# Kernel tuning notes

Measured on AMD Instinct MI355X. Metric: run time of the kernel, lower is better.

Reference implementation:

```python
import jax, jax.numpy as jnp
import numpy as np

N = 50000
E = 800000
D_IN = 128
D_HID = 128
D_EMB = 128
N_CLS = 3
EPS = 0.0  # GINConv default eps, not trainable here
LRELU_SLOPE = 0.2


def setup_inputs() -> dict:
    key = jax.random.key(0)
    ks = jax.random.split(key, 12)
    x = jax.random.normal(ks[0], (N, D_IN), dtype=jnp.float32)
    edge_index = jax.random.randint(ks[1], (2, E), 0, N, dtype=jnp.int64)
    node_label = jnp.zeros((10000, 1, N_CLS), dtype=jnp.float32)
    node_index = jax.random.randint(ks[2], (10000,), 0, N, dtype=jnp.int64)
    def lin(k, fan_in, fan_out):
        kw, kb = jax.random.split(k)
        bound = 1.0 / np.sqrt(fan_in)
        W = jax.random.uniform(kw, (fan_out, fan_in), minval=-bound, maxval=bound, dtype=jnp.float32)
        b = jax.random.uniform(kb, (fan_out,), minval=-bound, maxval=bound, dtype=jnp.float32)
        return W, b
    W1, b1 = lin(ks[3], D_IN, D_HID)
    W2, b2 = lin(ks[4], D_HID, D_HID)
    W3, b3 = lin(ks[5], D_HID, D_EMB)
    Wout, bout = lin(ks[6], D_EMB, N_CLS)
    return {"x": x, "edge_index": edge_index, "node_label": node_label,
            "node_index": node_index, "W1": W1, "b1": b1, "W2": W2, "b2": b2,
            "W3": W3, "b3": b3, "Wout": Wout, "bout": bout}


def gin_conv(x, src, dst, W, b):
    # h = Linear(x); out = relu(scatter_add(h[src] -> dst) + (1+eps)*h)
    h = x @ W.T + b                                   # [N, F_out]
    agg = jax.ops.segment_sum(h[src], dst, num_segments=N)
    return jax.nn.relu(agg + (1.0 + EPS) * h)


def leaky_relu(x):
    return jnp.where(x >= 0, x, LRELU_SLOPE * x)


def reference(x, edge_index, node_label, node_index, W1, b1, W2, b2, W3, b3, Wout, bout):
    src, dst = edge_index[0], edge_index[1]
    h = leaky_relu(gin_conv(x, src, dst, W1, b1))
    h = leaky_relu(gin_conv(h, src, dst, W2, b2))
    h = leaky_relu(gin_conv(h, src, dst, W3, b3))
    x_embed = h                                       # [N, D_EMB]
    output = h @ Wout.T + bout                        # [N, N_CLS]
    node_output = output[node_index]                  # [M, N_CLS]
    ypred = jnp.argmax(output, axis=1)                # [N]
    y_nodepred = ypred[node_index]                    # [M]
    return (x_embed, node_output, ypred, y_nodepred)
```

## Files before the change

### kernel.cpp

```cpp
#include <hip/hip_runtime.h>

#define NN 50000
#define EE 800000
#define D 128
#define NCLS 3
#define MIDX 10000
#define NB 196
#define CHUNK 4096
#define HIST_WGS 98
#define CONV_WGS 25000

typedef unsigned int uint32;
typedef unsigned short ushort16;
typedef __attribute__((ext_vector_type(8))) short short8;
typedef __attribute__((ext_vector_type(4))) float f32x4;

__device__ __forceinline__ ushort16 f2bf(float f) {
    uint32 u = __float_as_uint(f);
    u = (u + 0x7fffu + ((u >> 16) & 1u)) >> 16;
    return (ushort16)u;
}
__device__ __forceinline__ float bflo(uint32 packed) {
    return __uint_as_float(packed << 16);
}
__device__ __forceinline__ float bfhi(uint32 packed) {
    return __uint_as_float(packed & 0xFFFF0000u);
}

__device__ __forceinline__ void gather_rows(const uint32* __restrict__ h,
                                            const int* __restrict__ esrc,
                                            int beg, int end, int lane,
                                            float& a0, float& a1) {
    int i = beg;
    for (; i + 16 <= end; i += 16) {
        int s[16];
        uint32 q[16];
#pragma unroll
        for (int k = 0; k < 16; ++k) s[k] = esrc[i + k];
#pragma unroll
        for (int k = 0; k < 16; ++k) q[k] = h[(long long)s[k] * (D / 2) + lane];
        float t0a = 0.f, t0b = 0.f, t1a = 0.f, t1b = 0.f;
#pragma unroll
        for (int k = 0; k < 16; k += 2) {
            t0a += bflo(q[k]);     t1a += bfhi(q[k]);
            t0b += bflo(q[k + 1]); t1b += bfhi(q[k + 1]);
        }
        a0 += t0a + t0b;
        a1 += t1a + t1b;
    }
    for (; i + 4 <= end; i += 4) {
        int s[4];
        uint32 q[4];
#pragma unroll
        for (int k = 0; k < 4; ++k) s[k] = esrc[i + k];
#pragma unroll
        for (int k = 0; k < 4; ++k) q[k] = h[(long long)s[k] * (D / 2) + lane];
        a0 += (bflo(q[0]) + bflo(q[1])) + (bflo(q[2]) + bflo(q[3]));
        a1 += (bfhi(q[0]) + bfhi(q[1])) + (bfhi(q[2]) + bfhi(q[3]));
    }
    for (; i < end; ++i) {
        const uint32 q = h[(long long)esrc[i] * (D / 2) + lane];
        a0 += bflo(q);
        a1 += bfhi(q);
    }
}


__global__ __launch_bounds__(256) void prep_hist(const float* __restrict__ x0,
                                                 const float* __restrict__ W1,
                                                 const float* __restrict__ W2,
                                                 const float* __restrict__ W3,
                                                 const int* __restrict__ dst,
                                                 ushort16* __restrict__ xbf,
                                                 ushort16* __restrict__ Wbf,
                                                 int* __restrict__ hpart) {
    const int t = threadIdx.x;
    if (blockIdx.x < CONV_WGS) {
        const int i = blockIdx.x * 256 + t;
        xbf[i] = f2bf(x0[i]);
        if (i < D * D) {
            Wbf[i] = f2bf(W1[i]);
            Wbf[i + D * D] = f2bf(W2[i]);
            Wbf[i + 2 * D * D] = f2bf(W3[i]);
        }
    } else {
        __shared__ int hcnt[256];
        const int b = blockIdx.x - CONV_WGS;
        hcnt[t] = 0;
        __syncthreads();
        const int e0 = b * 8192;
        const int e1 = (e0 + 8192 < EE) ? e0 + 8192 : EE;
        for (int s = e0 + t; s < e1; s += 256) atomicAdd(&hcnt[dst[s] >> 8], 1);
        __syncthreads();
        hpart[b * 256 + t] = hcnt[t];
    }
}

__global__ void coarse_scan(const int* __restrict__ hpart, int* __restrict__ bstart,
                            int* __restrict__ bcursor, int* __restrict__ rowptr) {
    __shared__ int s[256];
    const int t = threadIdx.x;
    int v = 0;
    if (t < NB)
        for (int w = 0; w < HIST_WGS; ++w) v += hpart[w * 256 + t];
    s[t] = v;
    __syncthreads();
    for (int off = 1; off < 256; off <<= 1) {
        const int add = (t >= off) ? s[t - off] : 0;
        __syncthreads();
        s[t] += add;
        __syncthreads();
    }
    const int excl = s[t] - v;
    if (t < NB) {
        bstart[t] = excl;
        bcursor[t * 16] = excl;
    }
    if (t == NB - 1) bstart[NB] = excl + v;
    if (t == 0) rowptr[NN] = EE;
}

__global__ __launch_bounds__(256) void fill_coarse(const int* __restrict__ src,
                                                   const int* __restrict__ dst,
                                                   int* __restrict__ bcursor,
                                                   int* __restrict__ espacked) {
    __shared__ int hcnt[256];
    __shared__ int hbase[256];
    const int t = threadIdx.x;
    const int e0 = blockIdx.x * CHUNK;
    const int e1 = (e0 + CHUNK < EE) ? e0 + CHUNK : EE;
    hcnt[t] = 0;
    __syncthreads();
    for (int s = e0 + t; s < e1; s += 256) atomicAdd(&hcnt[dst[s] >> 8], 1);
    __syncthreads();
    if (t < NB) {
        const int c = hcnt[t];
        hbase[t] = c ? atomicAdd(&bcursor[t * 16], c) : 0;
    }
    hcnt[t] = 0;
    __syncthreads();
    for (int s = e0 + t; s < e1; s += 256) {
        const int d = dst[s];
        const int b = d >> 8;
        const int r = atomicAdd(&hcnt[b], 1);
        espacked[hbase[b] + r] = (src[s] << 8) | (d & 255);
    }
}

__global__ __launch_bounds__(256) void bucket_scatter(const int* __restrict__ espacked,
                                                      const int* __restrict__ bstart,
                                                      int* __restrict__ rowptr,
                                                      int* __restrict__ esrc) {
    __shared__ int cnt[256];
    __shared__ int sc[256];
    __shared__ int cur[256];
    const int b = blockIdx.x;
    const int t = threadIdx.x;
    const int n0 = b * 256;
    const int seg0 = bstart[b];
    const int seg1 = bstart[b + 1];
    cnt[t] = 0;
    __syncthreads();
    for (int s = seg0 + t; s < seg1; s += 256) atomicAdd(&cnt[espacked[s] & 255], 1);
    __syncthreads();
    const int v = cnt[t];
    sc[t] = v;
    __syncthreads();
    for (int off = 1; off < 256; off <<= 1) {
        const int add = (t >= off) ? sc[t - off] : 0;
        __syncthreads();
        sc[t] += add;
        __syncthreads();
    }
    const int excl = seg0 + sc[t] - v;
    if (n0 + t < NN) rowptr[n0 + t] = excl;
    cur[t] = excl;
    __syncthreads();
    for (int s = seg0 + t; s < seg1; s += 256) {
        const int p = espacked[s];
        const int pos = atomicAdd(&cur[p & 255], 1);
        esrc[pos] = p >> 8;
    }
}


__global__ __launch_bounds__(256) void linear_mfma(const ushort16* __restrict__ x,
                                                   const ushort16* __restrict__ Wbf,
                                                   const float* __restrict__ bias,
                                                   ushort16* __restrict__ h) {
    const int wave = threadIdx.x >> 6;
    const int lane = threadIdx.x & 63;
    const int m0 = blockIdx.x * 64 + wave * 16;
    if (m0 >= NN) return;
    const int lr = lane & 15;
    const int lk = (lane >> 4) * 8;

    f32x4 acc[8] = {};
#pragma unroll
    for (int k4 = 0; k4 < 4; ++k4) {
        const int kb = k4 * 32 + lk;
        const short8 af = *(const short8*)(x + (long long)(m0 + lr) * D + kb);
#pragma unroll
        for (int nt = 0; nt < 8; ++nt) {
            const short8 bfrag = *(const short8*)(Wbf + (nt * 16 + lr) * D + kb);
            acc[nt] = __builtin_amdgcn_mfma_f32_16x16x32_bf16(af, bfrag, acc[nt], 0, 0, 0);
        }
    }
    const int rbase = m0 + (lane >> 4) * 4;
#pragma unroll
    for (int nt = 0; nt < 8; ++nt) {
        const int f = nt * 16 + lr;
        const float bb = bias[f];
#pragma unroll
        for (int r = 0; r < 4; ++r)
            h[(long long)(rbase + r) * D + f] = f2bf(acc[nt][r] + bb);
    }
}


__global__ __launch_bounds__(256) void agg_linear(const uint32* __restrict__ h,
                                                  const int* __restrict__ rowptr,
                                                  const int* __restrict__ esrc,
                                                  const ushort16* __restrict__ Wbf,
                                                  const float* __restrict__ bias,
                                                  ushort16* __restrict__ hnext) {
    __shared__ uint32 xs[16][68];
    const int wave = threadIdx.x >> 6;
    const int lane = threadIdx.x & 63;
    const int m0 = blockIdx.x * 16;

#pragma unroll
    for (int j = 0; j < 4; ++j) {
        const int row = wave * 4 + j;
        const int node = __builtin_amdgcn_readfirstlane(m0 + row);
        const int beg = rowptr[node];
        const int end = rowptr[node + 1];
        const uint32 p = h[(long long)node * (D / 2) + lane];
        float acc0 = bflo(p), acc1 = bfhi(p);
        gather_rows(h, esrc, beg, end, lane, acc0, acc1);
        xs[row][lane] = ((uint32)f2bf(fmaxf(acc1, 0.f)) << 16) |
                        (uint32)f2bf(fmaxf(acc0, 0.f));
    }
    __syncthreads();

    const int lr = lane & 15;
    const int lk = (lane >> 4) * 8;
    f32x4 acc[2] = {};
#pragma unroll
    for (int k4 = 0; k4 < 4; ++k4) {
        const int kb = k4 * 32 + lk;
        const short8 af = *(const short8*)&xs[lr][kb >> 1];
#pragma unroll
        for (int f = 0; f < 2; ++f) {
            const int ft = wave * 2 + f;
            const short8 bfrag = *(const short8*)(Wbf + (ft * 16 + lr) * D + kb);
            acc[f] = __builtin_amdgcn_mfma_f32_16x16x32_bf16(af, bfrag, acc[f], 0, 0, 0);
        }
    }
    const int rbase = m0 + (lane >> 4) * 4;
#pragma unroll
    for (int f = 0; f < 2; ++f) {
        const int col = (wave * 2 + f) * 16 + lr;
        const float bb = bias[col];
#pragma unroll
        for (int r = 0; r < 4; ++r)
            hnext[(long long)(rbase + r) * D + col] = f2bf(acc[f][r] + bb);
    }
}


__global__ __launch_bounds__(256) void agg_head(const uint32* __restrict__ h,
                                                const int* __restrict__ rowptr,
                                                const int* __restrict__ esrc,
                                                float* __restrict__ xe,
                                                const float* __restrict__ Wout,
                                                const float* __restrict__ bout,
                                                float* __restrict__ logits,
                                                float* __restrict__ ypred) {
    const int wave = threadIdx.x >> 6;
    const int lane = threadIdx.x & 63;
    const int node = __builtin_amdgcn_readfirstlane(blockIdx.x * 4 + wave);
    if (node >= NN) return;
    const int beg = rowptr[node];
    const int end = rowptr[node + 1];
    const uint32 p = h[(long long)node * (D / 2) + lane];
    float acc0 = bflo(p), acc1 = bfhi(p);
    gather_rows(h, esrc, beg, end, lane, acc0, acc1);
    const float r0 = fmaxf(acc0, 0.f);
    const float r1 = fmaxf(acc1, 0.f);
    float2 r;
    r.x = r0;
    r.y = r1;
    ((float2*)(xe + (long long)node * D))[lane] = r;

    const float2 w0 = ((const float2*)(Wout + 0 * D))[lane];
    const float2 w1 = ((const float2*)(Wout + 1 * D))[lane];
    const float2 w2 = ((const float2*)(Wout + 2 * D))[lane];
    float l0 = r0 * w0.x + r1 * w0.y;
    float l1 = r0 * w1.x + r1 * w1.y;
    float l2 = r0 * w2.x + r1 * w2.y;
#pragma unroll
    for (int off = 32; off > 0; off >>= 1) {
        l0 += __shfl_xor(l0, off, 64);
        l1 += __shfl_xor(l1, off, 64);
        l2 += __shfl_xor(l2, off, 64);
    }
    if (lane == 0) {
        l0 += bout[0]; l1 += bout[1]; l2 += bout[2];
        logits[node * 3 + 0] = l0;
        logits[node * 3 + 1] = l1;
        logits[node * 3 + 2] = l2;
        int best = 0;
        float bv = l0;
        if (l1 > bv) { bv = l1; best = 1; }
        if (l2 > bv) { bv = l2; best = 2; }
        ypred[node] = (float)best;
    }
}

__global__ void gather_out(const float* __restrict__ logits, const float* __restrict__ ypred,
                           const int* __restrict__ nidx, float* __restrict__ node_out,
                           float* __restrict__ y_nodepred) {
    const int m = blockIdx.x * blockDim.x + threadIdx.x;
    if (m >= MIDX) return;
    const int n = nidx[m];
    node_out[m * 3 + 0] = logits[n * 3 + 0];
    node_out[m * 3 + 1] = logits[n * 3 + 1];
    node_out[m * 3 + 2] = logits[n * 3 + 2];
    y_nodepred[m] = ypred[n];
}

extern "C" void kernel_launch(void* const* d_in, const int* in_sizes, int n_in,
                              void* d_out, int out_size, void* d_ws, size_t ws_size,
                              hipStream_t stream) {
    const float* x0 = (const float*)d_in[0];
    const int* ei = (const int*)d_in[1];
    const int* src = ei;
    const int* dst = ei + EE;
    const int* nidx = (const int*)d_in[3];
    const float* W1 = (const float*)d_in[4];
    const float* b1 = (const float*)d_in[5];
    const float* W2 = (const float*)d_in[6];
    const float* b2 = (const float*)d_in[7];
    const float* W3 = (const float*)d_in[8];
    const float* b3 = (const float*)d_in[9];
    const float* Wout = (const float*)d_in[10];
    const float* bout = (const float*)d_in[11];

    char* ws = (char*)d_ws;
    ushort16* xbf  = (ushort16*)ws;
    ushort16* hbuf = xbf + (long long)NN * D;
    ushort16* Wbf  = hbuf + (long long)NN * D;
    float* logits  = (float*)(Wbf + 3 * D * D);
    int* rowptr    = (int*)(logits + (long long)NN * NCLS);
    int* hpart     = rowptr + NN + 4;
    int* bstart    = hpart + HIST_WGS * 256;
    int* bcursor   = bstart + 256;
    int* espacked  = bcursor + NB * 16 + 12;
    int* esrc      = espacked + EE;

    float* out = (float*)d_out;
    float* xe       = out;
    float* node_out = out + (long long)NN * D;
    float* yp       = node_out + MIDX * NCLS;
    float* ynp      = yp + NN;

    prep_hist<<<CONV_WGS + HIST_WGS, 256, 0, stream>>>(x0, W1, W2, W3, dst, xbf, Wbf, hpart);
    coarse_scan<<<1, 256, 0, stream>>>(hpart, bstart, bcursor, rowptr);
    fill_coarse<<<(EE + CHUNK - 1) / CHUNK, 256, 0, stream>>>(src, dst, bcursor, espacked);
    bucket_scatter<<<NB, 256, 0, stream>>>(espacked, bstart, rowptr, esrc);

    linear_mfma<<<(NN + 63) / 64, 256, 0, stream>>>(xbf, Wbf, b1, hbuf);
    agg_linear<<<NN / 16, 256, 0, stream>>>((const uint32*)hbuf, rowptr, esrc,
                                            Wbf + (long long)D * D, b2, xbf);
    agg_linear<<<NN / 16, 256, 0, stream>>>((const uint32*)xbf, rowptr, esrc,
                                            Wbf + 2LL * D * D, b3, hbuf);
    agg_head<<<(NN + 3) / 4, 256, 0, stream>>>((const uint32*)hbuf, rowptr, esrc,
                                               xe, Wout, bout, logits, yp);
    gather_out<<<(MIDX + 255) / 256, 256, 0, stream>>>(logits, yp, nidx, node_out, ynp);
}
```

Before: 193.2 us.

## Split wave halves across edges with 8-byte gathers; fuse input bf16 conversion into GEMM

```diff
diff --git a/kernel.cpp b/kernel.cpp
--- a/kernel.cpp
+++ b/kernel.cpp
@@ -8,7 +8,7 @@
 #define NB 196
 #define CHUNK 4096
 #define HIST_WGS 98
-#define CONV_WGS 25000
+#define WCONV_WGS 64
 
 typedef unsigned int uint32;
 typedef unsigned short ushort16;
@@ -27,65 +27,63 @@
     return __uint_as_float(packed & 0xFFFF0000u);
 }
 
-__device__ __forceinline__ void gather_rows(const uint32* __restrict__ h,
-                                            const int* __restrict__ esrc,
-                                            int beg, int end, int lane,
-                                            float& a0, float& a1) {
+__device__ __forceinline__ void gather_rows_paired(const uint32* __restrict__ h,
+                                                   const int* __restrict__ esrc,
+                                                   int beg, int end, int fl, int half,
+                                                   float& a0, float& a1, float& a2, float& a3) {
     int i = beg;
     for (; i + 16 <= end; i += 16) {
-        int s[16];
-        uint32 q[16];
-#pragma unroll
-        for (int k = 0; k < 16; ++k) s[k] = esrc[i + k];
-#pragma unroll
-        for (int k = 0; k < 16; ++k) q[k] = h[(long long)s[k] * (D / 2) + lane];
-        float t0a = 0.f, t0b = 0.f, t1a = 0.f, t1b = 0.f;
-#pragma unroll
-        for (int k = 0; k < 16; k += 2) {
-            t0a += bflo(q[k]);     t1a += bfhi(q[k]);
-            t0b += bflo(q[k + 1]); t1b += bfhi(q[k + 1]);
-        }
-        a0 += t0a + t0b;
-        a1 += t1a + t1b;
-    }
-    for (; i + 4 <= end; i += 4) {
+        int s[8];
+        uint2 q[8];
+#pragma unroll
+        for (int k = 0; k < 8; ++k) s[k] = esrc[i + 2 * k + half];
+#pragma unroll
+        for (int k = 0; k < 8; ++k) q[k] = *(const uint2*)(h + (long long)s[k] * (D / 2) + 2 * fl);
+#pragma unroll
+        for (int k = 0; k < 8; ++k) {
+            a0 += bflo(q[k].x); a1 += bfhi(q[k].x);
+            a2 += bflo(q[k].y); a3 += bfhi(q[k].y);
+        }
+    }
+    for (; i + 8 <= end; i += 8) {
         int s[4];
-        uint32 q[4];
-#pragma unroll
-        for (int k = 0; k < 4; ++k) s[k] = esrc[i + k];
-#pragma unroll
-        for (int k = 0; k < 4; ++k) q[k] = h[(long long)s[k] * (D / 2) + lane];
-        a0 += (bflo(q[0]) + bflo(q[1])) + (bflo(q[2]) + bflo(q[3]));
-        a1 += (bfhi(q[0]) + bfhi(q[1])) + (bfhi(q[2]) + bfhi(q[3]));
-    }
-    for (; i < end; ++i) {
-        const uint32 q = h[(long long)esrc[i] * (D / 2) + lane];
-        a0 += bflo(q);
-        a1 += bfhi(q);
-    }
-}
-
-
-__global__ __launch_bounds__(256) void prep_hist(const float* __restrict__ x0,
-                                                 const float* __restrict__ W1,
+        uint2 q[4];
+#pragma unroll
+        for (int k = 0; k < 4; ++k) s[k] = esrc[i + 2 * k + half];
+#pragma unroll
+        for (int k = 0; k < 4; ++k) q[k] = *(const uint2*)(h + (long long)s[k] * (D / 2) + 2 * fl);
+#pragma unroll
+        for (int k = 0; k < 4; ++k) {
+            a0 += bflo(q[k].x); a1 += bfhi(q[k].x);
+            a2 += bflo(q[k].y); a3 += bfhi(q[k].y);
+        }
+    }
+    for (; i < end; i += 2) {
+        const int n = i + half;
+        if (n < end) {
+            const uint2 q = *(const uint2*)(h + (long long)esrc[n] * (D / 2) + 2 * fl);
+            a0 += bflo(q.x); a1 += bfhi(q.x);
+            a2 += bflo(q.y); a3 += bfhi(q.y);
+        }
+    }
+}
+
+
+__global__ __launch_bounds__(256) void prep_hist(const float* __restrict__ W1,
                                                  const float* __restrict__ W2,
                                                  const float* __restrict__ W3,
                                                  const int* __restrict__ dst,
-                                                 ushort16* __restrict__ xbf,
                                                  ushort16* __restrict__ Wbf,
                                                  int* __restrict__ hpart) {
     const int t = threadIdx.x;
-    if (blockIdx.x < CONV_WGS) {
+    if (blockIdx.x < WCONV_WGS) {
         const int i = blockIdx.x * 256 + t;
-        xbf[i] = f2bf(x0[i]);
-        if (i < D * D) {
-            Wbf[i] = f2bf(W1[i]);
-            Wbf[i + D * D] = f2bf(W2[i]);
-            Wbf[i + 2 * D * D] = f2bf(W3[i]);
-        }
+        Wbf[i] = f2bf(W1[i]);
+        Wbf[i + D * D] = f2bf(W2[i]);
+        Wbf[i + 2 * D * D] = f2bf(W3[i]);
     } else {
         __shared__ int hcnt[256];
-        const int b = blockIdx.x - CONV_WGS;
+        const int b = blockIdx.x - WCONV_WGS;
         hcnt[t] = 0;
         __syncthreads();
         const int e0 = b * 8192;
@@ -184,10 +182,10 @@
 }
 
 
-__global__ __launch_bounds__(256) void linear_mfma(const ushort16* __restrict__ x,
-                                                   const ushort16* __restrict__ Wbf,
-                                                   const float* __restrict__ bias,
-                                                   ushort16* __restrict__ h) {
+__global__ __launch_bounds__(256) void linear_mfma_f32(const float* __restrict__ x,
+                                                       const ushort16* __restrict__ Wbf,
+                                                       const float* __restrict__ bias,
+                                                       ushort16* __restrict__ h) {
     const int wave = threadIdx.x >> 6;
     const int lane = threadIdx.x & 63;
     const int m0 = blockIdx.x * 64 + wave * 16;
@@ -199,7 +197,14 @@
 #pragma unroll
     for (int k4 = 0; k4 < 4; ++k4) {
         const int kb = k4 * 32 + lk;
-        const short8 af = *(const short8*)(x + (long long)(m0 + lr) * D + kb);
+        const float4* xp = (const float4*)(x + (long long)(m0 + lr) * D + kb);
+        const float4 a0 = xp[0];
+        const float4 a1 = xp[1];
+        short8 af;
+        af[0] = (short)f2bf(a0.x); af[1] = (short)f2bf(a0.y);
+        af[2] = (short)f2bf(a0.z); af[3] = (short)f2bf(a0.w);
+        af[4] = (short)f2bf(a1.x); af[5] = (short)f2bf(a1.y);
+        af[6] = (short)f2bf(a1.z); af[7] = (short)f2bf(a1.w);
 #pragma unroll
         for (int nt = 0; nt < 8; ++nt) {
             const short8 bfrag = *(const short8*)(Wbf + (nt * 16 + lr) * D + kb);
@@ -224,9 +229,11 @@
                                                   const ushort16* __restrict__ Wbf,
                                                   const float* __restrict__ bias,
                                                   ushort16* __restrict__ hnext) {
-    __shared__ uint32 xs[16][68];
+    __shared__ uint32 xs[16][76];
     const int wave = threadIdx.x >> 6;
     const int lane = threadIdx.x & 63;
+    const int fl = lane & 31;
+    const int half = lane >> 5;
     const int m0 = blockIdx.x * 16;
 
 #pragma unroll
@@ -235,11 +242,22 @@
         const int node = __builtin_amdgcn_readfirstlane(m0 + row);
         const int beg = rowptr[node];
         const int end = rowptr[node + 1];
-        const uint32 p = h[(long long)node * (D / 2) + lane];
-        float acc0 = bflo(p), acc1 = bfhi(p);
-        gather_rows(h, esrc, beg, end, lane, acc0, acc1);
-        xs[row][lane] = ((uint32)f2bf(fmaxf(acc1, 0.f)) << 16) |
-                        (uint32)f2bf(fmaxf(acc0, 0.f));
+        float a0 = 0.f, a1 = 0.f, a2 = 0.f, a3 = 0.f;
+        if (half == 0) {
+            const uint2 sp = *(const uint2*)(h + (long long)node * (D / 2) + 2 * fl);
+            a0 = bflo(sp.x); a1 = bfhi(sp.x); a2 = bflo(sp.y); a3 = bfhi(sp.y);
+        }
+        gather_rows_paired(h, esrc, beg, end, fl, half, a0, a1, a2, a3);
+        a0 += __shfl_xor(a0, 32, 64);
+        a1 += __shfl_xor(a1, 32, 64);
+        a2 += __shfl_xor(a2, 32, 64);
+        a3 += __shfl_xor(a3, 32, 64);
+        if (half == 0) {
+            uint2 w;
+            w.x = ((uint32)f2bf(fmaxf(a1, 0.f)) << 16) | (uint32)f2bf(fmaxf(a0, 0.f));
+            w.y = ((uint32)f2bf(fmaxf(a3, 0.f)) << 16) | (uint32)f2bf(fmaxf(a2, 0.f));
+            *(uint2*)&xs[row][2 * fl] = w;
+        }
     }
     __syncthreads();
 
@@ -279,26 +297,38 @@
                                                 float* __restrict__ ypred) {
     const int wave = threadIdx.x >> 6;
     const int lane = threadIdx.x & 63;
+    const int fl = lane & 31;
+    const int half = lane >> 5;
     const int node = __builtin_amdgcn_readfirstlane(blockIdx.x * 4 + wave);
     if (node >= NN) return;
     const int beg = rowptr[node];
     const int end = rowptr[node + 1];
-    const uint32 p = h[(long long)node * (D / 2) + lane];
-    float acc0 = bflo(p), acc1 = bfhi(p);
-    gather_rows(h, esrc, beg, end, lane, acc0, acc1);
-    const float r0 = fmaxf(acc0, 0.f);
-    const float r1 = fmaxf(acc1, 0.f);
-    float2 r;
-    r.x = r0;
-    r.y = r1;
-    ((float2*)(xe + (long long)node * D))[lane] = r;
-
-    const float2 w0 = ((const float2*)(Wout + 0 * D))[lane];
-    const float2 w1 = ((const float2*)(Wout + 1 * D))[lane];
-    const float2 w2 = ((const float2*)(Wout + 2 * D))[lane];
-    float l0 = r0 * w0.x + r1 * w0.y;
-    float l1 = r0 * w1.x + r1 * w1.y;
-    float l2 = r0 * w2.x + r1 * w2.y;
+    float a0 = 0.f, a1 = 0.f, a2 = 0.f, a3 = 0.f;
+    if (half == 0) {
+        const uint2 sp = *(const uint2*)(h + (long long)node * (D / 2) + 2 * fl);
+        a0 = bflo(sp.x); a1 = bfhi(sp.x); a2 = bflo(sp.y); a3 = bfhi(sp.y);
+    }
+    gather_rows_paired(h, esrc, beg, end, fl, half, a0, a1, a2, a3);
+    a0 += __shfl_xor(a0, 32, 64);
+    a1 += __shfl_xor(a1, 32, 64);
+    a2 += __shfl_xor(a2, 32, 64);
+    a3 += __shfl_xor(a3, 32, 64);
+    const float r0 = fmaxf(a0, 0.f);
+    const float r1 = fmaxf(a1, 0.f);
+    const float r2 = fmaxf(a2, 0.f);
+    const float r3 = fmaxf(a3, 0.f);
+    if (half == 0) {
+        float4 r;
+        r.x = r0; r.y = r1; r.z = r2; r.w = r3;
+        *(float4*)(xe + (long long)node * D + 4 * fl) = r;
+    }
+
+    const float4 w0 = *(const float4*)(Wout + 0 * D + 4 * fl);
+    const float4 w1 = *(const float4*)(Wout + 1 * D + 4 * fl);
+    const float4 w2 = *(const float4*)(Wout + 2 * D + 4 * fl);
+    float l0 = (half == 0) ? (r0 * w0.x + r1 * w0.y + r2 * w0.z + r3 * w0.w) : 0.f;
+    float l1 = (half == 0) ? (r0 * w1.x + r1 * w1.y + r2 * w1.z + r3 * w1.w) : 0.f;
+    float l2 = (half == 0) ? (r0 * w2.x + r1 * w2.y + r2 * w2.z + r3 * w2.w) : 0.f;
 #pragma unroll
     for (int off = 32; off > 0; off >>= 1) {
         l0 += __shfl_xor(l0, off, 64);
@@ -348,9 +378,9 @@
     const float* bout = (const float*)d_in[11];
 
     char* ws = (char*)d_ws;
-    ushort16* xbf  = (ushort16*)ws;
-    ushort16* hbuf = xbf + (long long)NN * D;
-    ushort16* Wbf  = hbuf + (long long)NN * D;
+    ushort16* hbuf = (ushort16*)ws;
+    ushort16* xbuf = hbuf + (long long)NN * D;
+    ushort16* Wbf  = xbuf + (long long)NN * D;
     float* logits  = (float*)(Wbf + 3 * D * D);
     int* rowptr    = (int*)(logits + (long long)NN * NCLS);
     int* hpart     = rowptr + NN + 4;
@@ -365,15 +395,15 @@
     float* yp       = node_out + MIDX * NCLS;
     float* ynp      = yp + NN;
 
-    prep_hist<<<CONV_WGS + HIST_WGS, 256, 0, stream>>>(x0, W1, W2, W3, dst, xbf, Wbf, hpart);
+    prep_hist<<<WCONV_WGS + HIST_WGS, 256, 0, stream>>>(W1, W2, W3, dst, Wbf, hpart);
     coarse_scan<<<1, 256, 0, stream>>>(hpart, bstart, bcursor, rowptr);
     fill_coarse<<<(EE + CHUNK - 1) / CHUNK, 256, 0, stream>>>(src, dst, bcursor, espacked);
     bucket_scatter<<<NB, 256, 0, stream>>>(espacked, bstart, rowptr, esrc);
 
-    linear_mfma<<<(NN + 63) / 64, 256, 0, stream>>>(xbf, Wbf, b1, hbuf);
+    linear_mfma_f32<<<(NN + 63) / 64, 256, 0, stream>>>(x0, Wbf, b1, hbuf);
     agg_linear<<<NN / 16, 256, 0, stream>>>((const uint32*)hbuf, rowptr, esrc,
-                                            Wbf + (long long)D * D, b2, xbf);
-    agg_linear<<<NN / 16, 256, 0, stream>>>((const uint32*)xbf, rowptr, esrc,
+                                            Wbf + (long long)D * D, b2, xbuf);
+    agg_linear<<<NN / 16, 256, 0, stream>>>((const uint32*)xbuf, rowptr, esrc,
                                             Wbf + 2LL * D * D, b3, hbuf);
     agg_head<<<(NN + 3) / 4, 256, 0, stream>>>((const uint32*)hbuf, rowptr, esrc,
                                                xe, Wout, bout, logits, yp);
```

New measurement: 200.0 us. +3.5%, slower.

## Fuse x bf16 conversion into first linear and merge it with coarse scan

Applied to the files above, without the earlier changes.

```diff
diff --git a/kernel.cpp b/kernel.cpp
--- a/kernel.cpp
+++ b/kernel.cpp
@@ -8,7 +8,8 @@
 #define NB 196
 #define CHUNK 4096
 #define HIST_WGS 98
-#define CONV_WGS 25000
+#define WCONV_WGS 64
+#define LIN1_WGS 782
 
 typedef unsigned int uint32;
 typedef unsigned short ushort16;
@@ -66,26 +67,21 @@
 }
 
 
-__global__ __launch_bounds__(256) void prep_hist(const float* __restrict__ x0,
-                                                 const float* __restrict__ W1,
+__global__ __launch_bounds__(256) void prep_hist(const float* __restrict__ W1,
                                                  const float* __restrict__ W2,
                                                  const float* __restrict__ W3,
                                                  const int* __restrict__ dst,
-                                                 ushort16* __restrict__ xbf,
                                                  ushort16* __restrict__ Wbf,
                                                  int* __restrict__ hpart) {
     const int t = threadIdx.x;
-    if (blockIdx.x < CONV_WGS) {
+    if (blockIdx.x < WCONV_WGS) {
         const int i = blockIdx.x * 256 + t;
-        xbf[i] = f2bf(x0[i]);
-        if (i < D * D) {
-            Wbf[i] = f2bf(W1[i]);
-            Wbf[i + D * D] = f2bf(W2[i]);
-            Wbf[i + 2 * D * D] = f2bf(W3[i]);
-        }
+        Wbf[i] = f2bf(W1[i]);
+        Wbf[i + D * D] = f2bf(W2[i]);
+        Wbf[i + 2 * D * D] = f2bf(W3[i]);
     } else {
         __shared__ int hcnt[256];
-        const int b = blockIdx.x - CONV_WGS;
+        const int b = blockIdx.x - WCONV_WGS;
         hcnt[t] = 0;
         __syncthreads();
         const int e0 = b * 8192;
@@ -96,29 +92,74 @@
     }
 }
 
-__global__ void coarse_scan(const int* __restrict__ hpart, int* __restrict__ bstart,
-                            int* __restrict__ bcursor, int* __restrict__ rowptr) {
-    __shared__ int s[256];
-    const int t = threadIdx.x;
-    int v = 0;
-    if (t < NB)
-        for (int w = 0; w < HIST_WGS; ++w) v += hpart[w * 256 + t];
-    s[t] = v;
-    __syncthreads();
-    for (int off = 1; off < 256; off <<= 1) {
-        const int add = (t >= off) ? s[t - off] : 0;
-        __syncthreads();
-        s[t] += add;
-        __syncthreads();
-    }
-    const int excl = s[t] - v;
-    if (t < NB) {
-        bstart[t] = excl;
-        bcursor[t * 16] = excl;
-    }
-    if (t == NB - 1) bstart[NB] = excl + v;
-    if (t == 0) rowptr[NN] = EE;
-}
+
+__global__ __launch_bounds__(256) void scan_linear1(const int* __restrict__ hpart,
+                                                    int* __restrict__ bstart,
+                                                    int* __restrict__ bcursor,
+                                                    int* __restrict__ rowptr,
+                                                    const float* __restrict__ x,
+                                                    const ushort16* __restrict__ Wbf,
+                                                    const float* __restrict__ bias,
+                                                    ushort16* __restrict__ h) {
+    if (blockIdx.x == 0) {
+        __shared__ int s[256];
+        const int t = threadIdx.x;
+        int v = 0;
+        if (t < NB)
+            for (int w = 0; w < HIST_WGS; ++w) v += hpart[w * 256 + t];
+        s[t] = v;
+        __syncthreads();
+        for (int off = 1; off < 256; off <<= 1) {
+            const int add = (t >= off) ? s[t - off] : 0;
+            __syncthreads();
+            s[t] += add;
+            __syncthreads();
+        }
+        const int excl = s[t] - v;
+        if (t < NB) {
+            bstart[t] = excl;
+            bcursor[t * 16] = excl;
+        }
+        if (t == NB - 1) bstart[NB] = excl + v;
+        if (t == 0) rowptr[NN] = EE;
+        return;
+    }
+    const int wave = threadIdx.x >> 6;
+    const int lane = threadIdx.x & 63;
+    const int m0 = (blockIdx.x - 1) * 64 + wave * 16;
+    if (m0 >= NN) return;
+    const int lr = lane & 15;
+    const int lk = (lane >> 4) * 8;
+
+    f32x4 acc[8] = {};
+#pragma unroll
+    for (int k4 = 0; k4 < 4; ++k4) {
+        const int kb = k4 * 32 + lk;
+        const float4* xp = (const float4*)(x + (long long)(m0 + lr) * D + kb);
+        const float4 a0 = xp[0];
+        const float4 a1 = xp[1];
+        short8 af;
+        af[0] = (short)f2bf(a0.x); af[1] = (short)f2bf(a0.y);
+        af[2] = (short)f2bf(a0.z); af[3] = (short)f2bf(a0.w);
+        af[4] = (short)f2bf(a1.x); af[5] = (short)f2bf(a1.y);
+        af[6] = (short)f2bf(a1.z); af[7] = (short)f2bf(a1.w);
+#pragma unroll
+        for (int nt = 0; nt < 8; ++nt) {
+            const short8 bfrag = *(const short8*)(Wbf + (nt * 16 + lr) * D + kb);
+            acc[nt] = __builtin_amdgcn_mfma_f32_16x16x32_bf16(af, bfrag, acc[nt], 0, 0, 0);
+        }
+    }
+    const int rbase = m0 + (lane >> 4) * 4;
+#pragma unroll
+    for (int nt = 0; nt < 8; ++nt) {
+        const int f = nt * 16 + lr;
+        const float bb = bias[f];
+#pragma unroll
+        for (int r = 0; r < 4; ++r)
+            h[(long long)(rbase + r) * D + f] = f2bf(acc[nt][r] + bb);
+    }
+}
+
 
 __global__ __launch_bounds__(256) void fill_coarse(const int* __restrict__ src,
                                                    const int* __restrict__ dst,
@@ -146,6 +187,7 @@
         espacked[hbase[b] + r] = (src[s] << 8) | (d & 255);
     }
 }
+
 
 __global__ __launch_bounds__(256) void bucket_scatter(const int* __restrict__ espacked,
                                                       const int* __restrict__ bstart,
@@ -180,40 +222,6 @@
         const int p = espacked[s];
         const int pos = atomicAdd(&cur[p & 255], 1);
         esrc[pos] = p >> 8;
-    }
-}
-
-
-__global__ __launch_bounds__(256) void linear_mfma(const ushort16* __restrict__ x,
-                                                   const ushort16* __restrict__ Wbf,
-                                                   const float* __restrict__ bias,
-                                                   ushort16* __restrict__ h) {
-    const int wave = threadIdx.x >> 6;
-    const int lane = threadIdx.x & 63;
-    const int m0 = blockIdx.x * 64 + wave * 16;
-    if (m0 >= NN) return;
-    const int lr = lane & 15;
-    const int lk = (lane >> 4) * 8;
-
-    f32x4 acc[8] = {};
-#pragma unroll
-    for (int k4 = 0; k4 < 4; ++k4) {
-        const int kb = k4 * 32 + lk;
-        const short8 af = *(const short8*)(x + (long long)(m0 + lr) * D + kb);
-#pragma unroll
-        for (int nt = 0; nt < 8; ++nt) {
-            const short8 bfrag = *(const short8*)(Wbf + (nt * 16 + lr) * D + kb);
-            acc[nt] = __builtin_amdgcn_mfma_f32_16x16x32_bf16(af, bfrag, acc[nt], 0, 0, 0);
-        }
-    }
-    const int rbase = m0 + (lane >> 4) * 4;
-#pragma unroll
-    for (int nt = 0; nt < 8; ++nt) {
-        const int f = nt * 16 + lr;
-        const float bb = bias[f];
-#pragma unroll
-        for (int r = 0; r < 4; ++r)
-            h[(long long)(rbase + r) * D + f] = f2bf(acc[nt][r] + bb);
     }
 }
 
@@ -318,6 +326,7 @@
     }
 }
 
+
 __global__ void gather_out(const float* __restrict__ logits, const float* __restrict__ ypred,
                            const int* __restrict__ nidx, float* __restrict__ node_out,
                            float* __restrict__ y_nodepred) {
@@ -348,9 +357,9 @@
     const float* bout = (const float*)d_in[11];
 
     char* ws = (char*)d_ws;
-    ushort16* xbf  = (ushort16*)ws;
-    ushort16* hbuf = xbf + (long long)NN * D;
-    ushort16* Wbf  = hbuf + (long long)NN * D;
+    ushort16* hbuf = (ushort16*)ws;
+    ushort16* xbuf = hbuf + (long long)NN * D;
+    ushort16* Wbf  = xbuf + (long long)NN * D;
     float* logits  = (float*)(Wbf + 3 * D * D);
     int* rowptr    = (int*)(logits + (long long)NN * NCLS);
     int* hpart     = rowptr + NN + 4;
@@ -365,15 +374,15 @@
     float* yp       = node_out + MIDX * NCLS;
     float* ynp      = yp + NN;
 
-    prep_hist<<<CONV_WGS + HIST_WGS, 256, 0, stream>>>(x0, W1, W2, W3, dst, xbf, Wbf, hpart);
-    coarse_scan<<<1, 256, 0, stream>>>(hpart, bstart, bcursor, rowptr);
+    prep_hist<<<WCONV_WGS + HIST_WGS, 256, 0, stream>>>(W1, W2, W3, dst, Wbf, hpart);
+    scan_linear1<<<1 + LIN1_WGS, 256, 0, stream>>>(hpart, bstart, bcursor, rowptr,
+                                                   x0, Wbf, b1, hbuf);
     fill_coarse<<<(EE + CHUNK - 1) / CHUNK, 256, 0, stream>>>(src, dst, bcursor, espacked);
     bucket_scatter<<<NB, 256, 0, stream>>>(espacked, bstart, rowptr, esrc);
 
-    linear_mfma<<<(NN + 63) / 64, 256, 0, stream>>>(xbf, Wbf, b1, hbuf);
     agg_linear<<<NN / 16, 256, 0, stream>>>((const uint32*)hbuf, rowptr, esrc,
-                                            Wbf + (long long)D * D, b2, xbf);
-    agg_linear<<<NN / 16, 256, 0, stream>>>((const uint32*)xbf, rowptr, esrc,
+                                            Wbf + (long long)D * D, b2, xbuf);
+    agg_linear<<<NN / 16, 256, 0, stream>>>((const uint32*)xbuf, rowptr, esrc,
                                             Wbf + 2LL * D * D, b3, hbuf);
     agg_head<<<(NN + 3) / 4, 256, 0, stream>>>((const uint32*)hbuf, rowptr, esrc,
                                                xe, Wout, bout, logits, yp);
```

Measured after the change: 180.3 us. 1.07x faster.
